# Performance work log

Hardware: AMD Instinct MI355X
Metric: run time of the kernel (lower is better)

The kernel has to match this reference:

```python
import jax, jax.numpy as jnp
import numpy as np

B, L, IN_DIMS = 256, 512, 64
UNITS, OUT_STEPS, OUT_DIMS = 256, 64, 32
KSIZE = 5


def setup_inputs() -> dict:
    key = jax.random.key(0)
    ks = jax.random.split(key, 14)
    s = lambda k, shp: jax.random.normal(k, shp, dtype=jnp.float32) * 0.05
    return {
        "inputs": jax.random.normal(ks[0], (B, L, IN_DIMS), dtype=jnp.float32),
        "conv_k": s(ks[1], (KSIZE, IN_DIMS, UNITS)),   # WIO layout
        "conv_b": s(ks[2], (UNITS,)),
        "enc_W": s(ks[3], (UNITS, 4 * UNITS)),          # kernel (input after CNN has UNITS channels)
        "enc_U": s(ks[4], (UNITS, 4 * UNITS)),          # recurrent kernel
        "enc_b": s(ks[5], (4 * UNITS,)),
        "cell_W": s(ks[6], (UNITS, 4 * UNITS)),
        "cell_U": s(ks[7], (UNITS, 4 * UNITS)),
        "cell_b": s(ks[8], (4 * UNITS,)),
        "fore_W": s(ks[9], (UNITS, OUT_DIMS)),
        "fore_b": s(ks[10], (OUT_DIMS,)),
        "back_W": s(ks[11], (UNITS, IN_DIMS)),
        "back_b": s(ks[12], (IN_DIMS,)),
    }


def _lstm_step(W, U, b, h, c, x_t):
    # Keras gate order: i, f, g(candidate), o
    z = x_t @ W + h @ U + b
    i, f, g, o = jnp.split(z, 4, axis=-1)
    c_new = jax.nn.sigmoid(f) * c + jax.nn.sigmoid(i) * jnp.tanh(g)
    h_new = jax.nn.sigmoid(o) * jnp.tanh(c_new)
    return h_new, c_new


def _forward(inputs, conv_k, conv_b, enc_W, enc_U, enc_b,
             cell_W, cell_U, cell_b, fore_W, fore_b, back_W, back_b):
    # Conv1D 'same', relu
    x = jax.lax.conv_general_dilated(
        inputs, conv_k, window_strides=(1,), padding="SAME",
        dimension_numbers=("NWC", "WIO", "NWC"))
    x = jax.nn.relu(x + conv_b)

    # Encoder LSTM (dropout inactive at inference)
    h0 = jnp.zeros((x.shape[0], UNITS), x.dtype)
    c0 = jnp.zeros((x.shape[0], UNITS), x.dtype)

    def enc_step(carry, x_t):
        h, c = carry
        h, c = _lstm_step(enc_W, enc_U, enc_b, h, c, x_t)
        return (h, c), h
    (h_T, c_T), seq = jax.lax.scan(enc_step, (h0, c0), jnp.swapaxes(x, 0, 1))
    backcast_seq = jnp.swapaxes(seq, 0, 1)  # [B, L, UNITS]

    def dec_step(carry, _):
        h, c = carry
        h, c = _lstm_step(cell_W, cell_U, cell_b, h, c, h)
        return (h, c), h
    _, outs = jax.lax.scan(dec_step, (h_T, c_T), None, length=OUT_STEPS)
    forecast_seq = jnp.swapaxes(outs, 0, 1)  # [B, OUT_STEPS, UNITS]

    forecast = forecast_seq @ fore_W + fore_b   # [B, OUT_STEPS, OUT_DIMS]
    backcast = backcast_seq @ back_W + back_b   # [B, L, IN_DIMS]
    return forecast, backcast


def reference(inputs, conv_k, conv_b, enc_W, enc_U, enc_b,
              cell_W, cell_U, cell_b, fore_W, fore_b, back_W, back_b):
    return _forward(inputs, conv_k, conv_b, enc_W, enc_U, enc_b,
                    cell_W, cell_U, cell_b, fore_W, fore_b, back_W, back_b)
```

## Files before the change

kernel.cpp:

```cpp
#include <hip/hip_runtime.h>
#include <stdint.h>

typedef unsigned short u16;
typedef __attribute__((ext_vector_type(8))) short bf16x8;
typedef __attribute__((ext_vector_type(4))) float fx4;

#define MFMA16(a, b, c) __builtin_amdgcn_mfma_f32_16x16x32_bf16((a), (b), (c), 0, 0, 0)

#define OFF_X      0u
#define OFF_CSAVE  0u
#define OFF_H      67108864u
#define OFF_ENCWT  142737408u
#define OFF_ENCUT  143261696u
#define OFF_CELLT  143785984u
#define OFF_CONVKT 144310272u
#define OFF_BWT    144474112u
#define OFF_FWT    144506880u
#define OFF_BAR    144523264u

__device__ __forceinline__ u16 f2bf(float f) {
    uint32_t u = __builtin_bit_cast(uint32_t, f);
    u += 0x7FFFu + ((u >> 16) & 1u);
    return (u16)(u >> 16);
}
__device__ __forceinline__ float sigm(float x) { return 1.0f / (1.0f + __expf(-x)); }
__device__ __forceinline__ float tanh_f(float x) { return 1.0f - 2.0f / (__expf(2.0f * x) + 1.0f); }

__device__ __forceinline__ void store_h_sc(const u16* p, uint32_t v) {
    asm volatile("global_store_short %0, %1, off sc0 sc1" :: "v"(p), "v"(v) : "memory");
}
__device__ __forceinline__ void vmcnt0() { asm volatile("s_waitcnt vmcnt(0)" ::: "memory"); }

__global__ void zero_kernel(unsigned char* ws) {
    int i = blockIdx.x * blockDim.x + threadIdx.x;
    uint32_t* h0 = (uint32_t*)(ws + OFF_H);
    for (int k = i; k < 32768; k += 16384) h0[k] = 0u;
    if (i < 256) ((uint32_t*)(ws + OFF_BAR))[i] = 0u;
}

__global__ void prep_kernel(const float* enc_W, const float* enc_U, const float* cell_W,
                            const float* cell_U, const float* conv_k, const float* back_W,
                            const float* fore_W, unsigned char* ws) {
    u16* encWt = (u16*)(ws + OFF_ENCWT);
    u16* encUt = (u16*)(ws + OFF_ENCUT);
    u16* cellT = (u16*)(ws + OFF_CELLT);
    u16* convKt = (u16*)(ws + OFF_CONVKT);
    u16* bwt = (u16*)(ws + OFF_BWT);
    u16* fwt = (u16*)(ws + OFF_FWT);
    int idx = blockIdx.x * blockDim.x + threadIdx.x;
    int stride = gridDim.x * blockDim.x;
    for (int i = idx; i < 262144; i += stride) {
        int n = i >> 8, k = i & 255;
        encWt[i] = f2bf(enc_W[k * 1024 + n]);
        encUt[i] = f2bf(enc_U[k * 1024 + n]);
        cellT[i] = f2bf(cell_W[k * 1024 + n] + cell_U[k * 1024 + n]);
    }
    for (int i = idx; i < 81920; i += stride) {
        int u = i / 320, rem = i - u * 320;
        convKt[i] = f2bf(conv_k[rem * 256 + u]);
    }
    for (int i = idx; i < 16384; i += stride) {
        int n = i >> 8, k = i & 255;
        bwt[i] = f2bf(back_W[k * 64 + n]);
    }
    for (int i = idx; i < 8192; i += stride) {
        int n = i >> 8, k = i & 255;
        fwt[i] = f2bf(fore_W[k * 32 + n]);
    }
}

__global__ __launch_bounds__(256) void conv_kernel(const float* __restrict__ in,
                                                   const float* __restrict__ conv_b,
                                                   unsigned char* ws) {
    const u16* kt = (const u16*)(ws + OFF_CONVKT);
    u16* xout = (u16*)(ws + OFF_X);
    int w = threadIdx.x >> 6, lane = threadIdx.x & 63;
    int m = lane & 15, q = lane >> 4;
    int mt = blockIdx.x * 4 + w;
    int r0 = mt * 16;
    int b = r0 >> 9;
    int l0 = r0 & 511;

    fx4 acc[16];
#pragma unroll
    for (int nt = 0; nt < 16; ++nt) acc[nt] = (fx4){0.f, 0.f, 0.f, 0.f};

#pragma unroll
    for (int s = 0; s < 10; ++s) {
        int k0 = s * 32 + q * 8;
        int kk = k0 >> 6, c = k0 & 63;
        int l2 = l0 + m + kk - 2;
        bf16x8 af = {0, 0, 0, 0, 0, 0, 0, 0};
        if (l2 >= 0 && l2 < 512) {
            const float* src = in + (((b << 9) + l2) << 6) + c;
            fx4 f0 = *(const fx4*)src;
            fx4 f1 = *(const fx4*)(src + 4);
            af[0] = (short)f2bf(f0[0]); af[1] = (short)f2bf(f0[1]);
            af[2] = (short)f2bf(f0[2]); af[3] = (short)f2bf(f0[3]);
            af[4] = (short)f2bf(f1[0]); af[5] = (short)f2bf(f1[1]);
            af[6] = (short)f2bf(f1[2]); af[7] = (short)f2bf(f1[3]);
        }
#pragma unroll
        for (int nt = 0; nt < 16; ++nt) {
            bf16x8 bf = *(const bf16x8*)(kt + (nt * 16 + m) * 320 + k0);
            acc[nt] = MFMA16(af, bf, acc[nt]);
        }
    }
#pragma unroll
    for (int nt = 0; nt < 16; ++nt) {
        int u = nt * 16 + m;
        float bias = conv_b[u];
#pragma unroll
        for (int r = 0; r < 4; ++r) {
            float v = acc[nt][r] + bias;
            v = v > 0.f ? v : 0.f;
            int row = r0 + q * 4 + r;
            xout[row * 256 + u] = f2bf(v);
        }
    }
}

__global__ __launch_bounds__(256, 1) void enc_kernel(const float* __restrict__ enc_b,
                                                     unsigned char* ws) {
    int tid = threadIdx.x;
    int w = tid >> 6, lane = tid & 63, m = lane & 15, q = lane >> 4;
    int bid = blockIdx.x;
    int g = bid & 15, p = bid >> 4;
    int b0 = g * 16;
    int un0 = p * 64 + w * 16;

    const u16* encWt = (const u16*)(ws + OFF_ENCWT);
    const u16* encUt = (const u16*)(ws + OFF_ENCUT);
    const u16* xbf = (const u16*)(ws + OFF_X);
    u16* H = (u16*)(ws + OFF_H);
    float* csave = (float*)(ws + OFF_CSAVE);
    int* bar = (int*)(ws + OFF_BAR + g * 64);

    bf16x8 wfrag[4][8], ufrag[4][8];
#pragma unroll
    for (int gi = 0; gi < 4; ++gi) {
#pragma unroll
        for (int s = 0; s < 8; ++s) {
            int n = gi * 256 + un0 + m;
            wfrag[gi][s] = *(const bf16x8*)(encWt + n * 256 + s * 32 + q * 8);
            ufrag[gi][s] = *(const bf16x8*)(encUt + n * 256 + s * 32 + q * 8);
        }
    }
    float bi[4], creg[4];
#pragma unroll
    for (int gi = 0; gi < 4; ++gi) bi[gi] = enc_b[gi * 256 + un0 + m];
    creg[0] = creg[1] = creg[2] = creg[3] = 0.f;

    const u16* xrow = xbf + (size_t)(b0 + m) * (512 * 256) + q * 8;

    for (int t = 0; t < 512; ++t) {
        bf16x8 xa[8];
        const u16* xA = xrow + (size_t)t * 256;
#pragma unroll
        for (int s = 0; s < 8; ++s) xa[s] = *(const bf16x8*)(xA + s * 32);
        fx4 acc[4];
#pragma unroll
        for (int gi = 0; gi < 4; ++gi) acc[gi] = (fx4){bi[gi], bi[gi], bi[gi], bi[gi]};
#pragma unroll
        for (int s = 0; s < 8; ++s) {
#pragma unroll
            for (int gi = 0; gi < 4; ++gi)
                acc[gi] = MFMA16(xa[s], wfrag[gi][s], acc[gi]);
        }

        if (lane == 0) {
            int tgt = 4 * t;
            while (__hip_atomic_load(bar, __ATOMIC_RELAXED, __HIP_MEMORY_SCOPE_AGENT) < tgt) {}
        }
        asm volatile("" ::: "memory");

        const u16* hA = H + (size_t)t * 65536 + (b0 + m) * 256 + q * 8;
        bf16x8 ha[8];
#pragma unroll
        for (int s = 0; s < 8; ++s) ha[s] = *(const bf16x8*)(hA + s * 32);
#pragma unroll
        for (int s = 0; s < 8; ++s) {
#pragma unroll
            for (int gi = 0; gi < 4; ++gi)
                acc[gi] = MFMA16(ha[s], ufrag[gi][s], acc[gi]);
        }

        const u16* hw = H + (size_t)(t + 1) * 65536 + un0 + m;
#pragma unroll
        for (int r = 0; r < 4; ++r) {
            float cv = sigm(acc[1][r]) * creg[r] + sigm(acc[0][r]) * tanh_f(acc[2][r]);
            creg[r] = cv;
            float hv = sigm(acc[3][r]) * tanh_f(cv);
            store_h_sc(hw + (b0 + q * 4 + r) * 256, (uint32_t)f2bf(hv));
        }
        vmcnt0();
        __syncthreads();
        if (tid == 0)
            __hip_atomic_fetch_add(bar, 1, __ATOMIC_RELAXED, __HIP_MEMORY_SCOPE_AGENT);
    }

#pragma unroll
    for (int r = 0; r < 4; ++r)
        csave[(b0 + q * 4 + r) * 256 + un0 + m] = creg[r];
}

__global__ __launch_bounds__(256, 1) void dec_kernel(const float* __restrict__ cell_b,
                                                     unsigned char* ws) {
    int tid = threadIdx.x;
    int w = tid >> 6, lane = tid & 63, m = lane & 15, q = lane >> 4;
    int bid = blockIdx.x;
    int g = bid & 15, p = bid >> 4;
    int b0 = g * 16;
    int un0 = p * 64 + w * 16;

    const u16* cellT = (const u16*)(ws + OFF_CELLT);
    u16* H = (u16*)(ws + OFF_H);
    const float* csave = (const float*)(ws + OFF_CSAVE);
    int* bar = (int*)(ws + OFF_BAR + g * 64);

    bf16x8 wfrag[4][8];
#pragma unroll
    for (int gi = 0; gi < 4; ++gi) {
#pragma unroll
        for (int s = 0; s < 8; ++s)
            wfrag[gi][s] = *(const bf16x8*)(cellT + (gi * 256 + un0 + m) * 256 + s * 32 + q * 8);
    }
    float bi[4], creg[4];
#pragma unroll
    for (int gi = 0; gi < 4; ++gi) bi[gi] = cell_b[gi * 256 + un0 + m];
#pragma unroll
    for (int r = 0; r < 4; ++r) creg[r] = csave[(b0 + q * 4 + r) * 256 + un0 + m];

    for (int t = 0; t < 64; ++t) {
        if (lane == 0) {
            int tgt = 2048 + 4 * t;
            while (__hip_atomic_load(bar, __ATOMIC_RELAXED, __HIP_MEMORY_SCOPE_AGENT) < tgt) {}
        }
        asm volatile("" ::: "memory");

        const u16* hA = H + (size_t)(512 + t) * 65536 + (b0 + m) * 256 + q * 8;
        bf16x8 ha[8];
#pragma unroll
        for (int s = 0; s < 8; ++s) ha[s] = *(const bf16x8*)(hA + s * 32);
        fx4 acc[4];
#pragma unroll
        for (int gi = 0; gi < 4; ++gi) acc[gi] = (fx4){bi[gi], bi[gi], bi[gi], bi[gi]};
#pragma unroll
        for (int s = 0; s < 8; ++s) {
#pragma unroll
            for (int gi = 0; gi < 4; ++gi)
                acc[gi] = MFMA16(ha[s], wfrag[gi][s], acc[gi]);
        }

        const u16* hw = H + (size_t)(513 + t) * 65536 + un0 + m;
#pragma unroll
        for (int r = 0; r < 4; ++r) {
            float cv = sigm(acc[1][r]) * creg[r] + sigm(acc[0][r]) * tanh_f(acc[2][r]);
            creg[r] = cv;
            float hv = sigm(acc[3][r]) * tanh_f(cv);
            store_h_sc(hw + (b0 + q * 4 + r) * 256, (uint32_t)f2bf(hv));
        }
        vmcnt0();
        __syncthreads();
        if (tid == 0)
            __hip_atomic_fetch_add(bar, 1, __ATOMIC_RELAXED, __HIP_MEMORY_SCOPE_AGENT);
    }
}

__global__ __launch_bounds__(256) void out_gemm(const u16* __restrict__ A,
                                                const u16* __restrict__ Bt,
                                                const float* __restrict__ bias,
                                                float* __restrict__ out,
                                                int ncols, int seqlen) {
    int w = threadIdx.x >> 6, lane = threadIdx.x & 63, m = lane & 15, q = lane >> 4;
    int mt = blockIdx.x * 4 + w;
    int s = mt >> 4;
    int b0 = (mt & 15) * 16;
    bf16x8 af[8];
    const u16* Arow = A + ((size_t)s * 256 + b0 + m) * 256 + q * 8;
#pragma unroll
    for (int ss = 0; ss < 8; ++ss) af[ss] = *(const bf16x8*)(Arow + ss * 32);
    int ntiles = ncols >> 4;
    for (int nt = 0; nt < ntiles; ++nt) {
        fx4 acc = (fx4){0.f, 0.f, 0.f, 0.f};
#pragma unroll
        for (int ss = 0; ss < 8; ++ss) {
            bf16x8 bf = *(const bf16x8*)(Bt + (nt * 16 + m) * 256 + ss * 32 + q * 8);
            acc = MFMA16(af[ss], bf, acc);
        }
        int col = nt * 16 + m;
        float bv = bias[col];
#pragma unroll
        for (int r = 0; r < 4; ++r) {
            int b = b0 + q * 4 + r;
            out[((size_t)b * seqlen + s) * ncols + col] = acc[r] + bv;
        }
    }
}

extern "C" void kernel_launch(void* const* d_in, const int* in_sizes, int n_in,
                              void* d_out, int out_size, void* d_ws, size_t ws_size,
                              hipStream_t stream) {
    const float* inputs = (const float*)d_in[0];
    const float* conv_k = (const float*)d_in[1];
    const float* conv_b = (const float*)d_in[2];
    const float* enc_W  = (const float*)d_in[3];
    const float* enc_U  = (const float*)d_in[4];
    const float* enc_b  = (const float*)d_in[5];
    const float* cell_W = (const float*)d_in[6];
    const float* cell_U = (const float*)d_in[7];
    const float* cell_b = (const float*)d_in[8];
    const float* fore_W = (const float*)d_in[9];
    const float* fore_b = (const float*)d_in[10];
    const float* back_W = (const float*)d_in[11];
    const float* back_b = (const float*)d_in[12];
    unsigned char* ws = (unsigned char*)d_ws;
    float* out = (float*)d_out;

    zero_kernel<<<64, 256, 0, stream>>>(ws);
    prep_kernel<<<1024, 256, 0, stream>>>(enc_W, enc_U, cell_W, cell_U, conv_k, back_W, fore_W, ws);
    conv_kernel<<<2048, 256, 0, stream>>>(inputs, conv_b, ws);
    enc_kernel<<<64, 256, 0, stream>>>(enc_b, ws);
    dec_kernel<<<64, 256, 0, stream>>>(cell_b, ws);

    const u16* H = (const u16*)(ws + OFF_H);
    out_gemm<<<2048, 256, 0, stream>>>(H + (size_t)1 * 65536, (const u16*)(ws + OFF_BWT),
                                       back_b, out + 524288, 64, 512);
    out_gemm<<<256, 256, 0, stream>>>(H + (size_t)513 * 65536, (const u16*)(ws + OFF_FWT),
                                      fore_b, out, 32, 64);
}
```

Measured before the change: 2.756 ms.

## Hoist encoder input projection and run each batch group's recurrence in one block

```diff
diff --git a/kernel.cpp b/kernel.cpp
--- a/kernel.cpp
+++ b/kernel.cpp
@@ -4,19 +4,25 @@
 typedef unsigned short u16;
 typedef __attribute__((ext_vector_type(8))) short bf16x8;
 typedef __attribute__((ext_vector_type(4))) float fx4;
+typedef __attribute__((ext_vector_type(2))) unsigned int u32x2;
 
 #define MFMA16(a, b, c) __builtin_amdgcn_mfma_f32_16x16x32_bf16((a), (b), (c), 0, 0, 0)
+#define KEEP(x) asm volatile("" : "+v"(x))
 
 #define OFF_X      0u
-#define OFF_CSAVE  0u
-#define OFF_H      67108864u
-#define OFF_ENCWT  142737408u
-#define OFF_ENCUT  143261696u
-#define OFF_CELLT  143785984u
-#define OFF_CONVKT 144310272u
-#define OFF_BWT    144474112u
-#define OFF_FWT    144506880u
-#define OFF_BAR    144523264u
+#define OFF_SEQ    0u
+#define OFF_ZRING  67108864u
+#define ZSLOT      33554432u
+#define OFF_FSEQ   67108864u
+#define OFF_ENCWT  134217728u
+#define OFF_ENCUT  134742016u
+#define OFF_CELLT  135266304u
+#define OFF_CONVKT 135790592u
+#define OFF_BWT    135954432u
+#define OFF_FWT    135987200u
+#define OFF_CSAVE  136003584u
+
+#define DYN_LDS (131072 + 16 * 264 * 2)
 
 __device__ __forceinline__ u16 f2bf(float f) {
     uint32_t u = __builtin_bit_cast(uint32_t, f);
@@ -25,18 +31,6 @@
 }
 __device__ __forceinline__ float sigm(float x) { return 1.0f / (1.0f + __expf(-x)); }
 __device__ __forceinline__ float tanh_f(float x) { return 1.0f - 2.0f / (__expf(2.0f * x) + 1.0f); }
-
-__device__ __forceinline__ void store_h_sc(const u16* p, uint32_t v) {
-    asm volatile("global_store_short %0, %1, off sc0 sc1" :: "v"(p), "v"(v) : "memory");
-}
-__device__ __forceinline__ void vmcnt0() { asm volatile("s_waitcnt vmcnt(0)" ::: "memory"); }
-
-__global__ void zero_kernel(unsigned char* ws) {
-    int i = blockIdx.x * blockDim.x + threadIdx.x;
-    uint32_t* h0 = (uint32_t*)(ws + OFF_H);
-    for (int k = i; k < 32768; k += 16384) h0[k] = 0u;
-    if (i < 256) ((uint32_t*)(ws + OFF_BAR))[i] = 0u;
-}
 
 __global__ void prep_kernel(const float* enc_W, const float* enc_U, const float* cell_W,
                             const float* cell_U, const float* conv_k, const float* back_W,
@@ -120,150 +114,277 @@
     }
 }
 
-__global__ __launch_bounds__(256, 1) void enc_kernel(const float* __restrict__ enc_b,
-                                                     unsigned char* ws) {
+__global__ __launch_bounds__(256) void zx_kernel(const float* __restrict__ enc_b,
+                                                 unsigned char* ws, int t0, int slot) {
+    const u16* xbf = (const u16*)(ws + OFF_X);
+    const u16* wt = (const u16*)(ws + OFF_ENCWT);
+    unsigned char* zc = ws + OFF_ZRING + (size_t)slot * ZSLOT;
+    int tid = threadIdx.x;
+    int nq = tid >> 6, lane = tid & 63, m = lane & 15, q = lane >> 4;
+    int bid = blockIdx.x;
+    int tp = bid >> 4, g = bid & 15;
+    int tl0 = tp * 2, b0 = g * 16;
+
+    fx4 acc[2][16];
+#pragma unroll
+    for (int ts = 0; ts < 2; ++ts)
+#pragma unroll
+        for (int ntl = 0; ntl < 16; ++ntl) acc[ts][ntl] = (fx4){0.f, 0.f, 0.f, 0.f};
+
+#pragma unroll
+    for (int s = 0; s < 8; ++s) {
+        bf16x8 a0 = *(const bf16x8*)(xbf + ((size_t)(b0 + m) * 512 + t0 + tl0) * 256 + s * 32 + q * 8);
+        bf16x8 a1 = *(const bf16x8*)(xbf + ((size_t)(b0 + m) * 512 + t0 + tl0 + 1) * 256 + s * 32 + q * 8);
+#pragma unroll
+        for (int ntl = 0; ntl < 16; ++ntl) {
+            bf16x8 bfg = *(const bf16x8*)(wt + (nq * 256 + ntl * 16 + m) * 256 + s * 32 + q * 8);
+            acc[0][ntl] = MFMA16(a0, bfg, acc[0][ntl]);
+            acc[1][ntl] = MFMA16(a1, bfg, acc[1][ntl]);
+        }
+    }
+
+    float eb[16];
+#pragma unroll
+    for (int ntl = 0; ntl < 16; ++ntl) eb[ntl] = enc_b[nq * 256 + ntl * 16 + m];
+
+#pragma unroll
+    for (int ts = 0; ts < 2; ++ts) {
+#pragma unroll
+        for (int ntl = 0; ntl < 16; ++ntl) {
+            int wp = ntl >> 2;
+            int tile = nq * 4 + (ntl & 3);
+            float v0 = acc[ts][ntl][0] + eb[ntl];
+            float v1 = acc[ts][ntl][1] + eb[ntl];
+            float v2 = acc[ts][ntl][2] + eb[ntl];
+            float v3 = acc[ts][ntl][3] + eb[ntl];
+            u32x2 d;
+            d.x = (uint32_t)f2bf(v0) | ((uint32_t)f2bf(v1) << 16);
+            d.y = (uint32_t)f2bf(v2) | ((uint32_t)f2bf(v3) << 16);
+            *(u32x2*)(zc + ((size_t)((tl0 + ts) * 16 + g) * 4 + wp) * 8192 + tile * 512 + lane * 8) = d;
+        }
+    }
+}
+
+__global__ __launch_bounds__(256, 1) void enc_kernel(unsigned char* ws, int t0, int slot) {
+    extern __shared__ char smem[];
+    u16* lds_w = (u16*)smem;
+    u16* lds_h = (u16*)(smem + 131072);
+
     int tid = threadIdx.x;
     int w = tid >> 6, lane = tid & 63, m = lane & 15, q = lane >> 4;
-    int bid = blockIdx.x;
-    int g = bid & 15, p = bid >> 4;
+    int g = blockIdx.x;
     int b0 = g * 16;
-    int un0 = p * 64 + w * 16;
-
-    const u16* encWt = (const u16*)(ws + OFF_ENCWT);
-    const u16* encUt = (const u16*)(ws + OFF_ENCUT);
-    const u16* xbf = (const u16*)(ws + OFF_X);
-    u16* H = (u16*)(ws + OFF_H);
+
+    const u16* Ut = (const u16*)(ws + OFF_ENCUT);
+    const unsigned char* zc = ws + OFF_ZRING + (size_t)slot * ZSLOT;
+    u16* seq = (u16*)(ws + OFF_SEQ);
     float* csave = (float*)(ws + OFF_CSAVE);
-    int* bar = (int*)(ws + OFF_BAR + g * 64);
-
-    bf16x8 wfrag[4][8], ufrag[4][8];
-#pragma unroll
-    for (int gi = 0; gi < 4; ++gi) {
-#pragma unroll
-        for (int s = 0; s < 8; ++s) {
-            int n = gi * 256 + un0 + m;
-            wfrag[gi][s] = *(const bf16x8*)(encWt + n * 256 + s * 32 + q * 8);
-            ufrag[gi][s] = *(const bf16x8*)(encUt + n * 256 + s * 32 + q * 8);
-        }
-    }
-    float bi[4], creg[4];
-#pragma unroll
-    for (int gi = 0; gi < 4; ++gi) bi[gi] = enc_b[gi * 256 + un0 + m];
-    creg[0] = creg[1] = creg[2] = creg[3] = 0.f;
-
-    const u16* xrow = xbf + (size_t)(b0 + m) * (512 * 256) + q * 8;
-
-    for (int t = 0; t < 512; ++t) {
-        bf16x8 xa[8];
-        const u16* xA = xrow + (size_t)t * 256;
-#pragma unroll
-        for (int s = 0; s < 8; ++s) xa[s] = *(const bf16x8*)(xA + s * 32);
-        fx4 acc[4];
-#pragma unroll
-        for (int gi = 0; gi < 4; ++gi) acc[gi] = (fx4){bi[gi], bi[gi], bi[gi], bi[gi]};
-#pragma unroll
-        for (int s = 0; s < 8; ++s) {
+
+    bf16x8 wf[16][6];
+#pragma unroll
+    for (int nt = 0; nt < 16; ++nt) {
+        int col = (nt >> 2) * 256 + w * 64 + (nt & 3) * 16 + m;
+#pragma unroll
+        for (int s = 0; s < 6; ++s) {
+            wf[nt][s] = *(const bf16x8*)(Ut + col * 256 + s * 32 + q * 8);
+            KEEP(wf[nt][s]);
+        }
+#pragma unroll
+        for (int ss = 0; ss < 2; ++ss) {
+            bf16x8 f = *(const bf16x8*)(Ut + col * 256 + (6 + ss) * 32 + q * 8);
+            *(bf16x8*)(lds_w + (size_t)((w * 32 + nt * 2 + ss) * 64 + lane) * 8) = f;
+        }
+    }
+
+    if (t0 == 0) {
+        uint32_t* h32 = (uint32_t*)lds_h;
+        for (int i = tid; i < 2112; i += 256) h32[i] = 0u;
+    } else {
+        int row = tid >> 4, u0 = (tid & 15) * 16;
+        const u16* src = seq + ((size_t)(b0 + row) * 512 + (t0 - 1)) * 256 + u0;
+        *(bf16x8*)(lds_h + row * 264 + u0) = *(const bf16x8*)src;
+        *(bf16x8*)(lds_h + row * 264 + u0 + 8) = *(const bf16x8*)(src + 8);
+    }
+    float c[16];
+    if (t0 == 0) {
+#pragma unroll
+        for (int i = 0; i < 16; ++i) c[i] = 0.f;
+    } else {
+        const float* cs = csave + ((size_t)(g * 4 + w) * 64 + lane) * 16;
+#pragma unroll
+        for (int jr = 0; jr < 16; jr += 4) {
+            fx4 cv = *(const fx4*)(cs + jr);
+            c[jr] = cv[0]; c[jr + 1] = cv[1]; c[jr + 2] = cv[2]; c[jr + 3] = cv[3];
+        }
+    }
+    __syncthreads();
+
+    for (int tl = 0; tl < 64; ++tl) {
+        bf16x8 ha[8];
+#pragma unroll
+        for (int s = 0; s < 8; ++s)
+            ha[s] = *(const bf16x8*)(lds_h + m * 264 + s * 32 + q * 8);
+        __syncthreads();
+
+        const unsigned char* zrow = zc + ((size_t)(tl * 16 + g) * 4 + w) * 8192 + lane * 8;
+
+#pragma unroll
+        for (int j = 0; j < 4; ++j) {
+            u32x2 zd[4];
 #pragma unroll
             for (int gi = 0; gi < 4; ++gi)
-                acc[gi] = MFMA16(xa[s], wfrag[gi][s], acc[gi]);
-        }
-
-        if (lane == 0) {
-            int tgt = 4 * t;
-            while (__hip_atomic_load(bar, __ATOMIC_RELAXED, __HIP_MEMORY_SCOPE_AGENT) < tgt) {}
-        }
-        asm volatile("" ::: "memory");
-
-        const u16* hA = H + (size_t)t * 65536 + (b0 + m) * 256 + q * 8;
-        bf16x8 ha[8];
-#pragma unroll
-        for (int s = 0; s < 8; ++s) ha[s] = *(const bf16x8*)(hA + s * 32);
-#pragma unroll
-        for (int s = 0; s < 8; ++s) {
-#pragma unroll
-            for (int gi = 0; gi < 4; ++gi)
-                acc[gi] = MFMA16(ha[s], ufrag[gi][s], acc[gi]);
-        }
-
-        const u16* hw = H + (size_t)(t + 1) * 65536 + un0 + m;
-#pragma unroll
-        for (int r = 0; r < 4; ++r) {
-            float cv = sigm(acc[1][r]) * creg[r] + sigm(acc[0][r]) * tanh_f(acc[2][r]);
-            creg[r] = cv;
-            float hv = sigm(acc[3][r]) * tanh_f(cv);
-            store_h_sc(hw + (b0 + q * 4 + r) * 256, (uint32_t)f2bf(hv));
-        }
-        vmcnt0();
+                zd[gi] = *(const u32x2*)(zrow + (gi * 4 + j) * 512);
+
+            fx4 acc[4];
+#pragma unroll
+            for (int gi = 0; gi < 4; ++gi) acc[gi] = (fx4){0.f, 0.f, 0.f, 0.f};
+#pragma unroll
+            for (int s = 0; s < 6; ++s)
+#pragma unroll
+                for (int gi = 0; gi < 4; ++gi)
+                    acc[gi] = MFMA16(ha[s], wf[gi * 4 + j][s], acc[gi]);
+#pragma unroll
+            for (int ss = 0; ss < 2; ++ss)
+#pragma unroll
+                for (int gi = 0; gi < 4; ++gi) {
+                    int nt = gi * 4 + j;
+                    bf16x8 lwf = *(const bf16x8*)(lds_w + (size_t)((w * 32 + nt * 2 + ss) * 64 + lane) * 8);
+                    acc[gi] = MFMA16(ha[6 + ss], lwf, acc[gi]);
+                }
+#pragma unroll
+            for (int r = 0; r < 4; ++r) {
+                uint32_t di = (r < 2) ? zd[0].x : zd[0].y;
+                uint32_t df = (r < 2) ? zd[1].x : zd[1].y;
+                uint32_t dg = (r < 2) ? zd[2].x : zd[2].y;
+                uint32_t dz = (r < 2) ? zd[3].x : zd[3].y;
+                float zi = __builtin_bit_cast(float, (r & 1) ? (di & 0xffff0000u) : (di << 16));
+                float zf = __builtin_bit_cast(float, (r & 1) ? (df & 0xffff0000u) : (df << 16));
+                float zg = __builtin_bit_cast(float, (r & 1) ? (dg & 0xffff0000u) : (dg << 16));
+                float zo = __builtin_bit_cast(float, (r & 1) ? (dz & 0xffff0000u) : (dz << 16));
+                float iv = acc[0][r] + zi, fv = acc[1][r] + zf;
+                float gv = acc[2][r] + zg, ov = acc[3][r] + zo;
+                float cv = sigm(fv) * c[j * 4 + r] + sigm(iv) * tanh_f(gv);
+                c[j * 4 + r] = cv;
+                lds_h[(q * 4 + r) * 264 + w * 64 + j * 16 + m] = f2bf(sigm(ov) * tanh_f(cv));
+            }
+        }
         __syncthreads();
-        if (tid == 0)
-            __hip_atomic_fetch_add(bar, 1, __ATOMIC_RELAXED, __HIP_MEMORY_SCOPE_AGENT);
-    }
-
-#pragma unroll
-    for (int r = 0; r < 4; ++r)
-        csave[(b0 + q * 4 + r) * 256 + un0 + m] = creg[r];
+
+        {
+            int row = tid >> 4, u0 = (tid & 15) * 16;
+            bf16x8 h0 = *(const bf16x8*)(lds_h + row * 264 + u0);
+            bf16x8 h1 = *(const bf16x8*)(lds_h + row * 264 + u0 + 8);
+            u16* dst = seq + ((size_t)(b0 + row) * 512 + t0 + tl) * 256 + u0;
+            *(bf16x8*)dst = h0;
+            *(bf16x8*)(dst + 8) = h1;
+        }
+    }
+
+    float* cs = csave + ((size_t)(g * 4 + w) * 64 + lane) * 16;
+#pragma unroll
+    for (int jr = 0; jr < 16; jr += 4)
+        *(fx4*)(cs + jr) = (fx4){c[jr], c[jr + 1], c[jr + 2], c[jr + 3]};
 }
 
 __global__ __launch_bounds__(256, 1) void dec_kernel(const float* __restrict__ cell_b,
                                                      unsigned char* ws) {
+    extern __shared__ char smem[];
+    u16* lds_w = (u16*)smem;
+    u16* lds_h = (u16*)(smem + 131072);
+
     int tid = threadIdx.x;
     int w = tid >> 6, lane = tid & 63, m = lane & 15, q = lane >> 4;
-    int bid = blockIdx.x;
-    int g = bid & 15, p = bid >> 4;
+    int g = blockIdx.x;
     int b0 = g * 16;
-    int un0 = p * 64 + w * 16;
-
-    const u16* cellT = (const u16*)(ws + OFF_CELLT);
-    u16* H = (u16*)(ws + OFF_H);
+
+    const u16* Ut = (const u16*)(ws + OFF_CELLT);
+    const u16* seq = (const u16*)(ws + OFF_SEQ);
+    u16* fseq = (u16*)(ws + OFF_FSEQ);
     const float* csave = (const float*)(ws + OFF_CSAVE);
-    int* bar = (int*)(ws + OFF_BAR + g * 64);
-
-    bf16x8 wfrag[4][8];
-#pragma unroll
-    for (int gi = 0; gi < 4; ++gi) {
+
+    bf16x8 wf[16][6];
+#pragma unroll
+    for (int nt = 0; nt < 16; ++nt) {
+        int col = (nt >> 2) * 256 + w * 64 + (nt & 3) * 16 + m;
+#pragma unroll
+        for (int s = 0; s < 6; ++s) {
+            wf[nt][s] = *(const bf16x8*)(Ut + col * 256 + s * 32 + q * 8);
+            KEEP(wf[nt][s]);
+        }
+#pragma unroll
+        for (int ss = 0; ss < 2; ++ss) {
+            bf16x8 f = *(const bf16x8*)(Ut + col * 256 + (6 + ss) * 32 + q * 8);
+            *(bf16x8*)(lds_w + (size_t)((w * 32 + nt * 2 + ss) * 64 + lane) * 8) = f;
+        }
+    }
+    float bi[16];
+#pragma unroll
+    for (int nt = 0; nt < 16; ++nt)
+        bi[nt] = cell_b[(nt >> 2) * 256 + w * 64 + (nt & 3) * 16 + m];
+
+    {
+        int row = tid >> 4, u0 = (tid & 15) * 16;
+        const u16* src = seq + ((size_t)(b0 + row) * 512 + 511) * 256 + u0;
+        *(bf16x8*)(lds_h + row * 264 + u0) = *(const bf16x8*)src;
+        *(bf16x8*)(lds_h + row * 264 + u0 + 8) = *(const bf16x8*)(src + 8);
+    }
+    float c[16];
+    {
+        const float* cs = csave + ((size_t)(g * 4 + w) * 64 + lane) * 16;
+#pragma unroll
+        for (int jr = 0; jr < 16; jr += 4) {
+            fx4 cv = *(const fx4*)(cs + jr);
+            c[jr] = cv[0]; c[jr + 1] = cv[1]; c[jr + 2] = cv[2]; c[jr + 3] = cv[3];
+        }
+    }
+    __syncthreads();
+
+    for (int t = 0; t < 64; ++t) {
+        bf16x8 ha[8];
 #pragma unroll
         for (int s = 0; s < 8; ++s)
-            wfrag[gi][s] = *(const bf16x8*)(cellT + (gi * 256 + un0 + m) * 256 + s * 32 + q * 8);
-    }
-    float bi[4], creg[4];
-#pragma unroll
-    for (int gi = 0; gi < 4; ++gi) bi[gi] = cell_b[gi * 256 + un0 + m];
-#pragma unroll
-    for (int r = 0; r < 4; ++r) creg[r] = csave[(b0 + q * 4 + r) * 256 + un0 + m];
-
-    for (int t = 0; t < 64; ++t) {
-        if (lane == 0) {
-            int tgt = 2048 + 4 * t;
-            while (__hip_atomic_load(bar, __ATOMIC_RELAXED, __HIP_MEMORY_SCOPE_AGENT) < tgt) {}
-        }
-        asm volatile("" ::: "memory");
-
-        const u16* hA = H + (size_t)(512 + t) * 65536 + (b0 + m) * 256 + q * 8;
-        bf16x8 ha[8];
-#pragma unroll
-        for (int s = 0; s < 8; ++s) ha[s] = *(const bf16x8*)(hA + s * 32);
-        fx4 acc[4];
-#pragma unroll
-        for (int gi = 0; gi < 4; ++gi) acc[gi] = (fx4){bi[gi], bi[gi], bi[gi], bi[gi]};
-#pragma unroll
-        for (int s = 0; s < 8; ++s) {
-#pragma unroll
-            for (int gi = 0; gi < 4; ++gi)
-                acc[gi] = MFMA16(ha[s], wfrag[gi][s], acc[gi]);
-        }
-
-        const u16* hw = H + (size_t)(513 + t) * 65536 + un0 + m;
-#pragma unroll
-        for (int r = 0; r < 4; ++r) {
-            float cv = sigm(acc[1][r]) * creg[r] + sigm(acc[0][r]) * tanh_f(acc[2][r]);
-            creg[r] = cv;
-            float hv = sigm(acc[3][r]) * tanh_f(cv);
-            store_h_sc(hw + (b0 + q * 4 + r) * 256, (uint32_t)f2bf(hv));
-        }
-        vmcnt0();
+            ha[s] = *(const bf16x8*)(lds_h + m * 264 + s * 32 + q * 8);
         __syncthreads();
-        if (tid == 0)
-            __hip_atomic_fetch_add(bar, 1, __ATOMIC_RELAXED, __HIP_MEMORY_SCOPE_AGENT);
+
+#pragma unroll
+        for (int j = 0; j < 4; ++j) {
+            fx4 acc[4];
+#pragma unroll
+            for (int gi = 0; gi < 4; ++gi) acc[gi] = (fx4){0.f, 0.f, 0.f, 0.f};
+#pragma unroll
+            for (int s = 0; s < 6; ++s)
+#pragma unroll
+                for (int gi = 0; gi < 4; ++gi)
+                    acc[gi] = MFMA16(ha[s], wf[gi * 4 + j][s], acc[gi]);
+#pragma unroll
+            for (int ss = 0; ss < 2; ++ss)
+#pragma unroll
+                for (int gi = 0; gi < 4; ++gi) {
+                    int nt = gi * 4 + j;
+                    bf16x8 lwf = *(const bf16x8*)(lds_w + (size_t)((w * 32 + nt * 2 + ss) * 64 + lane) * 8);
+                    acc[gi] = MFMA16(ha[6 + ss], lwf, acc[gi]);
+                }
+#pragma unroll
+            for (int r = 0; r < 4; ++r) {
+                float iv = acc[0][r] + bi[0 * 4 + j];
+                float fv = acc[1][r] + bi[1 * 4 + j];
+                float gv = acc[2][r] + bi[2 * 4 + j];
+                float ov = acc[3][r] + bi[3 * 4 + j];
+                float cv = sigm(fv) * c[j * 4 + r] + sigm(iv) * tanh_f(gv);
+                c[j * 4 + r] = cv;
+                lds_h[(q * 4 + r) * 264 + w * 64 + j * 16 + m] = f2bf(sigm(ov) * tanh_f(cv));
+            }
+        }
+        __syncthreads();
+
+        {
+            int row = tid >> 4, u0 = (tid & 15) * 16;
+            bf16x8 h0 = *(const bf16x8*)(lds_h + row * 264 + u0);
+            bf16x8 h1 = *(const bf16x8*)(lds_h + row * 264 + u0 + 8);
+            u16* dst = fseq + ((size_t)(b0 + row) * 64 + t) * 256 + u0;
+            *(bf16x8*)dst = h0;
+            *(bf16x8*)(dst + 8) = h1;
+        }
     }
 }
 
@@ -271,13 +392,13 @@
                                                 const u16* __restrict__ Bt,
                                                 const float* __restrict__ bias,
                                                 float* __restrict__ out,
-                                                int ncols, int seqlen) {
+                                                int ncols, int seqT) {
     int w = threadIdx.x >> 6, lane = threadIdx.x & 63, m = lane & 15, q = lane >> 4;
     int mt = blockIdx.x * 4 + w;
     int s = mt >> 4;
     int b0 = (mt & 15) * 16;
     bf16x8 af[8];
-    const u16* Arow = A + ((size_t)s * 256 + b0 + m) * 256 + q * 8;
+    const u16* Arow = A + ((size_t)(b0 + m) * seqT + s) * 256 + q * 8;
 #pragma unroll
     for (int ss = 0; ss < 8; ++ss) af[ss] = *(const bf16x8*)(Arow + ss * 32);
     int ntiles = ncols >> 4;
@@ -293,7 +414,7 @@
 #pragma unroll
         for (int r = 0; r < 4; ++r) {
             int b = b0 + q * 4 + r;
-            out[((size_t)b * seqlen + s) * ncols + col] = acc[r] + bv;
+            out[((size_t)b * seqT + s) * ncols + col] = acc[r] + bv;
         }
     }
 }
@@ -317,15 +438,27 @@
     unsigned char* ws = (unsigned char*)d_ws;
     float* out = (float*)d_out;
 
-    zero_kernel<<<64, 256, 0, stream>>>(ws);
+    hipFuncSetAttribute((const void*)enc_kernel,
+                        hipFuncAttributeMaxDynamicSharedMemorySize, DYN_LDS);
+    hipFuncSetAttribute((const void*)dec_kernel,
+                        hipFuncAttributeMaxDynamicSharedMemorySize, DYN_LDS);
+
     prep_kernel<<<1024, 256, 0, stream>>>(enc_W, enc_U, cell_W, cell_U, conv_k, back_W, fore_W, ws);
     conv_kernel<<<2048, 256, 0, stream>>>(inputs, conv_b, ws);
-    enc_kernel<<<64, 256, 0, stream>>>(enc_b, ws);
-    dec_kernel<<<64, 256, 0, stream>>>(cell_b, ws);
-
-    const u16* H = (const u16*)(ws + OFF_H);
-    out_gemm<<<2048, 256, 0, stream>>>(H + (size_t)1 * 65536, (const u16*)(ws + OFF_BWT),
+
+    zx_kernel<<<512, 256, 0, stream>>>(enc_b, ws, 0, 0);
+    zx_kernel<<<512, 256, 0, stream>>>(enc_b, ws, 64, 1);
+    for (int k = 0; k < 8; ++k) {
+        if (k >= 2) {  }
+        enc_kernel<<<16, 256, DYN_LDS, stream>>>(ws, k * 64, k & 1);
+        if (k + 2 < 8)
+            zx_kernel<<<512, 256, 0, stream>>>(enc_b, ws, (k + 2) * 64, (k + 2) & 1);
+    }
+
+    dec_kernel<<<16, 256, DYN_LDS, stream>>>(cell_b, ws);
+
+    out_gemm<<<2048, 256, 0, stream>>>((const u16*)(ws + OFF_SEQ), (const u16*)(ws + OFF_BWT),
                                        back_b, out + 524288, 64, 512);
-    out_gemm<<<256, 256, 0, stream>>>(H + (size_t)513 * 65536, (const u16*)(ws + OFF_FWT),
+    out_gemm<<<256, 256, 0, stream>>>((const u16*)(ws + OFF_FSEQ), (const u16*)(ws + OFF_FWT),
                                       fore_b, out, 32, 64);
 }
```

Result: slower. 6.062 ms (+120.0%).
